# Kernel tuning notes

Hardware: AMD Instinct MI355X
Metric: run time of the kernel (lower is better)

Reference implementation:

```python
import jax, jax.numpy as jnp
import numpy as np

B, I, O, DEG = 16384, 1024, 1024, 8

def setup_inputs() -> dict:
    key = jax.random.key(0)
    kx, kc = jax.random.split(key)
    x = jax.random.normal(kx, (B, I), dtype=jnp.float32)
    std = 1.0 / (I * (DEG + 1))
    cheby_coeffs = jax.random.normal(kc, (I, O, DEG + 1), dtype=jnp.float32) * std
    return {"x": x, "cheby_coeffs": cheby_coeffs}


def reference(x, cheby_coeffs):
    # Chebyshev basis: T_d(tanh(x)) = cos(d * acos(tanh(x)))
    deg = cheby_coeffs.shape[-1]
    arange = jnp.arange(deg, dtype=x.dtype)  # (D+1,)
    theta = jnp.arccos(jnp.tanh(x))          # (B, I)
    basis = jnp.cos(theta[:, :, None] * arange)  # (B, I, D+1)
    y = jnp.einsum('bid,iod->bo', basis, cheby_coeffs)
    return y
```

## Files before the change

### kernel.cpp

```cpp
#include <hip/hip_runtime.h>
#include <hip/hip_bf16.h>


#define WSCALE 4096.0f
#define INV_WSCALE (1.0f/4096.0f)

typedef _Float16 f16;
typedef __fp16   hf2  __attribute__((ext_vector_type(2)));
typedef _Float16 f16x2v __attribute__((ext_vector_type(2)));
typedef _Float16 f16x8 __attribute__((ext_vector_type(8)));
typedef float    f32x4 __attribute__((ext_vector_type(4)));
typedef float    f32x4u __attribute__((ext_vector_type(4), aligned(4)));
typedef float    f32x2u __attribute__((ext_vector_type(2), aligned(4)));
typedef float    f32x16 __attribute__((ext_vector_type(16)));

union F16x8u { hf2 h2[4]; f16x8 v8; };

__global__ __launch_bounds__(256) void prep_kernel(const float* __restrict__ x,
                                                   const float* __restrict__ cc,
                                                   f16* __restrict__ t2,
                                                   f16* __restrict__ wt,
                                                   float* __restrict__ bias) {
  __shared__ char smem[18432];
  const int bid = blockIdx.x;
  const int t   = threadIdx.x;

  if (bid < 1024) {
    f16* s16 = (f16*)smem;
    const int u    = bid & 3;
    const int ncol = (bid >> 2) & 7;
    const int ic   = bid >> 5;
    const int i2   = t >> 4;
    const int o2   = t & 15;
    const int i0   = i2 * 2, o0 = o2 * 2;
    const int h    = i0 >> 4;
    const int kl   = (i0 >> 3) & 1;
    const int e    = i0 & 7;

    float va[2][18];
#pragma unroll
    for (int ii = 0; ii < 2; ++ii) {
      const float* g = cc + ((size_t)(ic * 32 + i0 + ii) * 1024
                             + (ncol * 128 + u * 32 + o0)) * 9;
      f32x4u a = *(const f32x4u*)(g);
      f32x4u b = *(const f32x4u*)(g + 4);
      f32x4u c4 = *(const f32x4u*)(g + 8);
      f32x4u d4 = *(const f32x4u*)(g + 12);
      f32x2u e2 = *(const f32x2u*)(g + 16);
#pragma unroll
      for (int j = 0; j < 4; ++j) { va[ii][j] = a[j]; va[ii][4 + j] = b[j];
                                    va[ii][8 + j] = c4[j]; va[ii][12 + j] = d4[j]; }
      va[ii][16] = e2[0]; va[ii][17] = e2[1];
    }

#pragma unroll
    for (int oo = 0; oo < 2; ++oo) {
      const int ol = o0 + oo;
      const int r  = ol & 15, q = ol >> 4;
      const int rk = (r >> 1) & 3;
      const int vsl = (kl * 2 + q) ^ rk;
      const int jj = h * 16 + r;
#pragma unroll
      for (int d = 0; d < 9; ++d) {
        f16x2v pv = { (f16)(va[0][oo * 9 + d] * WSCALE),
                      (f16)(va[1][oo * 9 + d] * WSCALE) };
        *(f16x2v*)(&s16[(d * 128 + jj * 4 + vsl) * 8 + e]) = pv;
      }
    }
    __syncthreads();

#pragma unroll
    for (int w = 0; w < 5; ++w) {
      int cidx = t + 256 * w;
      if (cidx < 1152) {
        f16x8 val = *(const f16x8*)(&s16[cidx * 8]);
        int d = cidx >> 7, rem = cidx & 127;
        *(f16x8*)(wt + (size_t)((d * 32 + ic) * 8 + ncol) * 4096 + u * 1024 + rem * 8) = val;
      }
    }
  } else if (bid < 1088) {
    float* red = (float*)smem;
    const int ol = t >> 4;
    const int sl = t & 15;
    const int o  = (bid - 1024) * 16 + ol;
    float s = 0.f;
    const float* p = cc + (size_t)(sl * 64) * 9216 + (size_t)o * 9;
#pragma unroll 4
    for (int i = 0; i < 64; ++i) s += p[(size_t)i * 9216];
    red[t] = s;
    __syncthreads();
    if (sl < 8) red[t] += red[t + 8];
    __syncthreads();
    if (sl < 4) red[t] += red[t + 4];
    __syncthreads();
    if (sl < 2) red[t] += red[t + 2];
    __syncthreads();
    if (sl == 0) bias[o] = red[t] + red[t + 1];
  } else {
    size_t gid = (size_t)(bid - 1088) * 256 + t;
    const float* p = x + gid * 8;
    f32x4 a = *(const f32x4*)p;
    f32x4 b = *(const f32x4*)(p + 4);
    float tf[8];
#pragma unroll
    for (int e = 0; e < 8; ++e) {
      float xx = (e < 4) ? a[e] : b[e - 4];
      tf[e] = 1.f - 2.f * __builtin_amdgcn_rcpf(__expf(2.f * xx) + 1.f);
    }
    F16x8u u;
#pragma unroll
    for (int q = 0; q < 4; ++q)
      u.h2[q] = __builtin_amdgcn_cvt_pkrtz(tf[2 * q], tf[2 * q + 1]);
    f16x8 v = u.v8 + u.v8;
    *(f16x8*)(t2 + gid * 8) = v;
  }
}

__global__ __launch_bounds__(256, 3) void cheby_gemm(const f16* __restrict__ t2g,
                                                     const f16* __restrict__ wt,
                                                     const float* __restrict__ bias,
                                                     float* __restrict__ out) {
  __shared__ f16 bbuf[5][4096];

  const int tid  = threadIdx.x;
  const int wid  = tid >> 6;
  const int lane = tid & 63;
  const int lr   = lane & 31;
  const int lh   = lane >> 5;
  const int wm   = wid >> 1;
  const int wn   = wid & 1;
  const int mrow = blockIdx.x >> 3;
  const int ncol = blockIdx.x & 7;
  const int m0   = mrow * 128 + wm * 64;
  const int n0   = ncol * 128 + wn * 64;
  const int rbase = wn * 2048 + ((lane & 15) * 4 + ((lane >> 4) ^ ((lane >> 1) & 3))) * 8;

  auto stage = [&](int cn, int dn, int slot) {
    const f16* src = wt + (size_t)(dn * 32 + cn) * 32768 + (size_t)ncol * 4096;
    __builtin_amdgcn_global_load_lds(
        (const __attribute__((address_space(1))) unsigned*)(src + tid * 8),
        (__attribute__((address_space(3))) unsigned*)(&bbuf[slot][wid * 512]),
        16, 0, 0);
    __builtin_amdgcn_global_load_lds(
        (const __attribute__((address_space(1))) unsigned*)(src + 2048 + tid * 8),
        (__attribute__((address_space(3))) unsigned*)(&bbuf[slot][wid * 512 + 2048]),
        16, 0, 0);
  };

  f32x16 acc[2][2];
#pragma unroll
  for (int a = 0; a < 2; ++a)
#pragma unroll
    for (int b = 0; b < 2; ++b)
#pragma unroll
      for (int j = 0; j < 16; ++j) acc[a][b][j] = 0.f;

  const f16x8 ones  = {(f16)1,(f16)1,(f16)1,(f16)1,(f16)1,(f16)1,(f16)1,(f16)1};
  const f16x8 half8 = {(f16)0.5f,(f16)0.5f,(f16)0.5f,(f16)0.5f,
                       (f16)0.5f,(f16)0.5f,(f16)0.5f,(f16)0.5f};
  f16x8 t2v[2][2], t2n[2][2];

  auto loadx = [&](int cn) {
#pragma unroll
    for (int mb = 0; mb < 2; ++mb)
#pragma unroll
      for (int h = 0; h < 2; ++h)
        t2n[mb][h] = *(const f16x8*)(t2g + (size_t)(m0 + mb * 32 + lr) * 1024
                                         + cn * 32 + h * 16 + lh * 8);
  };

#define REC(NEW, S1, S2)                                                       \
  _Pragma("unroll") for (int mb = 0; mb < 2; ++mb)                             \
    _Pragma("unroll") for (int h = 0; h < 2; ++h)                              \
      NEW[mb][h] = __builtin_elementwise_fma(t2v[mb][h], S1[mb][h], -S2[mb][h]);

#define LB(BD, SLOT)                                                           \
  {                                                                            \
    const f16* bb = &bbuf[0][0] + (SLOT) * 4096 + rbase;                       \
    BD[0][0] = *(const f16x8*)&bb[0];    BD[0][1] = *(const f16x8*)&bb[512];   \
    BD[1][0] = *(const f16x8*)&bb[1024]; BD[1][1] = *(const f16x8*)&bb[1536];  \
  }

#define M8(AF, BD)                                                             \
  {                                                                            \
    _Pragma("unroll") for (int nb = 0; nb < 2; ++nb)                           \
      _Pragma("unroll") for (int mb = 0; mb < 2; ++mb) {                       \
        acc[mb][nb] = __builtin_amdgcn_mfma_f32_32x32x16_f16(AF[mb][0], BD[nb][0], \
                                                             acc[mb][nb], 0, 0, 0); \
        acc[mb][nb] = __builtin_amdgcn_mfma_f32_32x32x16_f16(AF[mb][1], BD[nb][1], \
                                                             acc[mb][nb], 0, 0, 0); \
      }                                                                        \
  }

#define ADOPT                                                                  \
  _Pragma("unroll") for (int mb = 0; mb < 2; ++mb)                             \
    _Pragma("unroll") for (int h = 0; h < 2; ++h) {                            \
      t2v[mb][h] = t2n[mb][h];                                                 \
      A1[mb][h]  = t2v[mb][h] * half8;                                         \
    }

#define VMB(N)                                                                 \
  asm volatile("s_waitcnt vmcnt(" #N ")" ::: "memory");                        \
  __builtin_amdgcn_s_barrier();

  f16x8 onesA[2][2];
#pragma unroll
  for (int mb = 0; mb < 2; ++mb)
#pragma unroll
    for (int h = 0; h < 2; ++h) onesA[mb][h] = ones;

  f16x8 bfA[2][2], bfB[2][2];
  f16x8 A1[2][2], A2[2][2], A3[2][2], A4[2][2], A5[2][2], A6[2][2], A7[2][2], A8[2][2];
  int s1 = 0, s2 = 1, s3 = 2, s4 = 3, s5 = 4;

  loadx(0);
  stage(0, 1, s1); stage(0, 2, s2); stage(0, 3, s3); stage(0, 4, s4);

  for (int c = 0; c < 31; ++c) {
    VMB(4)
    LB(bfA, s1)
    ADOPT
    stage(c, 5, s5);
    loadx(c + 1);
    LB(bfB, s2)
    M8(A1, bfA)

    VMB(8) stage(c, 6, s1); LB(bfA, s3) REC(A2, A1, onesA) M8(A2, bfB)
    VMB(8) stage(c, 7, s2); LB(bfB, s4) REC(A3, A2, A1)    M8(A3, bfA)
    VMB(8) stage(c, 8, s3); LB(bfA, s5) REC(A4, A3, A2)    M8(A4, bfB)
    VMB(4) stage(c + 1, 1, s4); LB(bfB, s1) REC(A5, A4, A3) M8(A5, bfA)
    VMB(4) stage(c + 1, 2, s5); LB(bfA, s2) REC(A6, A5, A4) M8(A6, bfB)
    VMB(4) stage(c + 1, 3, s1); LB(bfB, s3) REC(A7, A6, A5) M8(A7, bfA)
    stage(c + 1, 4, s2);
    REC(A8, A7, A6) M8(A8, bfB)

    { int n1 = s4, n2 = s5, n3 = s1, n4 = s2, n5 = s3;
      s1 = n1; s2 = n2; s3 = n3; s4 = n4; s5 = n5; }
  }

  {
    VMB(4)
    LB(bfA, s1)
    ADOPT
    stage(31, 5, s5);
    LB(bfB, s2)
    M8(A1, bfA)

    VMB(4) stage(31, 6, s1); LB(bfA, s3) REC(A2, A1, onesA) M8(A2, bfB)
    VMB(4) stage(31, 7, s2); LB(bfB, s4) REC(A3, A2, A1)    M8(A3, bfA)
    VMB(4) stage(31, 8, s3); LB(bfA, s5) REC(A4, A3, A2)    M8(A4, bfB)
    VMB(4) LB(bfB, s1) REC(A5, A4, A3) M8(A5, bfA)
    VMB(2) LB(bfA, s2) REC(A6, A5, A4) M8(A6, bfB)
    VMB(0) LB(bfB, s3) REC(A7, A6, A5) M8(A7, bfA)
    REC(A8, A7, A6) M8(A8, bfB)
  }
#undef REC
#undef LB
#undef M8
#undef ADOPT
#undef VMB

  float bno[2];
  bno[0] = bias[n0 + lr];
  bno[1] = bias[n0 + 32 + lr];
#pragma unroll
  for (int mb = 0; mb < 2; ++mb)
#pragma unroll
    for (int nb = 0; nb < 2; ++nb)
#pragma unroll
      for (int j = 0; j < 16; ++j) {
        int row = m0 + mb * 32 + 4 * lh + (j & 3) + 8 * (j >> 2);
        int col = n0 + nb * 32 + lr;
        out[(size_t)row * 1024 + col] = acc[mb][nb][j] * INV_WSCALE + bno[nb];
      }
}

__global__ __launch_bounds__(512, 2) void cheby_gemm_fb(const float* __restrict__ x,
                                                        const f16* __restrict__ wt,
                                                        float* __restrict__ out) {
  __shared__ f16 bbuf[18][4096];
  const int tid  = threadIdx.x;
  const int wid  = tid >> 6;
  const int lane = tid & 63;
  const int lr   = lane & 31;
  const int lh   = lane >> 5;
  const int wm   = wid >> 1;
  const int wn   = wid & 1;
  const int mrow = blockIdx.x >> 3;
  const int ncol = blockIdx.x & 7;
  const int m0   = mrow * 256 + wm * 64;
  const int n0   = ncol * 128 + wn * 64;
  const int rbase = wn * 2048 + ((lane & 15) * 4 + ((lane >> 4) ^ ((lane >> 1) & 3))) * 8;

  auto stage = [&](int cn, int dn, int buf) {
    const f16* src = wt + (size_t)(dn * 32 + cn) * 32768 + (size_t)ncol * 4096;
    __builtin_amdgcn_global_load_lds(
        (const __attribute__((address_space(1))) unsigned*)(src + tid * 8),
        (__attribute__((address_space(3))) unsigned*)(&bbuf[buf][wid * 512]),
        16, 0, 0);
  };
  auto stage9 = [&](int cn, int b0) {
#pragma unroll
    for (int d = 0; d < 9; ++d) stage(cn, d, b0 + d);
  };

  f32x16 acc[2][2];
#pragma unroll
  for (int a = 0; a < 2; ++a)
#pragma unroll
    for (int b = 0; b < 2; ++b)
#pragma unroll
      for (int j = 0; j < 16; ++j) acc[a][b][j] = 0.f;

  const f16x8 ones  = {(f16)1,(f16)1,(f16)1,(f16)1,(f16)1,(f16)1,(f16)1,(f16)1};
  const f16x8 half8 = {(f16)0.5f,(f16)0.5f,(f16)0.5f,(f16)0.5f,
                       (f16)0.5f,(f16)0.5f,(f16)0.5f,(f16)0.5f};
  f16x8 t2v[2][2], t2n[2][2];
  f32x4 xf[2][2][2];

  auto loadx = [&](int cn) {
#pragma unroll
    for (int mb = 0; mb < 2; ++mb)
#pragma unroll
      for (int h = 0; h < 2; ++h) {
        const float* p = x + (size_t)(m0 + mb * 32 + lr) * 1024 + cn * 32 + h * 16 + lh * 8;
        xf[mb][h][0] = *(const f32x4*)p;
        xf[mb][h][1] = *(const f32x4*)(p + 4);
      }
  };
  auto dotanh = [&]() {
#pragma unroll
    for (int mb = 0; mb < 2; ++mb)
#pragma unroll
      for (int h = 0; h < 2; ++h) {
        float tf[8];
#pragma unroll
        for (int e = 0; e < 8; ++e) {
          float xx = (e < 4) ? xf[mb][h][0][e] : xf[mb][h][1][e - 4];
          tf[e] = 1.f - 2.f * __builtin_amdgcn_rcpf(__expf(2.f * xx) + 1.f);
        }
        F16x8u u;
#pragma unroll
        for (int q = 0; q < 4; ++q)
          u.h2[q] = __builtin_amdgcn_cvt_pkrtz(tf[2 * q], tf[2 * q + 1]);
        t2n[mb][h] = u.v8 + u.v8;
      }
  };

#define REC(NEW, S1, S2)                                                       \
  _Pragma("unroll") for (int mb = 0; mb < 2; ++mb)                             \
    _Pragma("unroll") for (int h = 0; h < 2; ++h)                              \
      NEW[mb][h] = __builtin_elementwise_fma(t2v[mb][h], S1[mb][h], -S2[mb][h]);
#define CLUSTER(AF, DIDX)                                                      \
  {                                                                            \
    const f16* bb = &bbuf[0][0] + sbase + (DIDX) * 4096 + rbase;               \
    f16x8 bf[2][2];                                                            \
    _Pragma("unroll") for (int nb = 0; nb < 2; ++nb)                           \
      _Pragma("unroll") for (int h = 0; h < 2; ++h)                            \
        bf[nb][h] = *(const f16x8*)&bb[nb * 1024 + h * 512];                   \
    _Pragma("unroll") for (int nb = 0; nb < 2; ++nb)                           \
      _Pragma("unroll") for (int mb = 0; mb < 2; ++mb) {                       \
        acc[mb][nb] = __builtin_amdgcn_mfma_f32_32x32x16_f16(AF[mb][0], bf[nb][0], \
                                                             acc[mb][nb], 0, 0, 0); \
        acc[mb][nb] = __builtin_amdgcn_mfma_f32_32x32x16_f16(AF[mb][1], bf[nb][1], \
                                                             acc[mb][nb], 0, 0, 0); \
      }                                                                        \
  }

  stage9(0, 0);
  loadx(0);
  dotanh();

  f16x8 onesA[2][2];
#pragma unroll
  for (int mb = 0; mb < 2; ++mb)
#pragma unroll
    for (int h = 0; h < 2; ++h) onesA[mb][h] = ones;

  for (int c = 0; c < 32; ++c) {
    const bool lastc = (c == 31);
    const int  sbase = (c & 1) * 36864;
    const int  nbase = (1 - (c & 1)) * 9;

    asm volatile("s_waitcnt vmcnt(8)" ::: "memory");
    __builtin_amdgcn_s_barrier();

    f16x8 A1[2][2], A2[2][2], A3[2][2], A4[2][2], A5[2][2], A6[2][2], A7[2][2], A8[2][2];
#pragma unroll
    for (int mb = 0; mb < 2; ++mb)
#pragma unroll
      for (int h = 0; h < 2; ++h) {
        t2v[mb][h] = t2n[mb][h];
        A1[mb][h]  = t2v[mb][h] * half8;
      }
    if (!lastc) { stage9(c + 1, nbase); loadx(c + 1); }

    CLUSTER(onesA, 0)
    CLUSTER(A1, 1)
    REC(A2, A1, onesA)  CLUSTER(A2, 2)
    REC(A3, A2, A1)     CLUSTER(A3, 3)
    REC(A4, A3, A2)     CLUSTER(A4, 4)
    REC(A5, A4, A3)     CLUSTER(A5, 5)
    REC(A6, A5, A4)     CLUSTER(A6, 6)
    REC(A7, A6, A5)     CLUSTER(A7, 7)
    REC(A8, A7, A6)     CLUSTER(A8, 8)
    if (!lastc) dotanh();
  }
#undef REC
#undef CLUSTER

#pragma unroll
  for (int mb = 0; mb < 2; ++mb)
#pragma unroll
    for (int nb = 0; nb < 2; ++nb)
#pragma unroll
      for (int j = 0; j < 16; ++j) {
        int row = m0 + mb * 32 + 4 * lh + (j & 3) + 8 * (j >> 2);
        int col = n0 + nb * 32 + lr;
        out[(size_t)row * 1024 + col] = acc[mb][nb][j] * INV_WSCALE;
      }
}

extern "C" void kernel_launch(void* const* d_in, const int* in_sizes, int n_in,
                              void* d_out, int out_size, void* d_ws, size_t ws_size,
                              hipStream_t stream) {
  const float* x  = (const float*)d_in[0];
  const float* cc = (const float*)d_in[1];
  f16*   wt   = (f16*)d_ws;
  f16*   t2   = (f16*)((char*)d_ws + 18874368);
  float* bias = (float*)((char*)d_ws + 52428800);
  float* out  = (float*)d_out;

  if (ws_size >= 52432896) {
    hipLaunchKernelGGL(prep_kernel, dim3(9280), dim3(256), 0, stream, x, cc, t2, wt, bias);
    hipLaunchKernelGGL(cheby_gemm, dim3(1024), dim3(256), 0, stream, t2, wt, bias, out);
  } else {
    hipLaunchKernelGGL(prep_kernel, dim3(1024), dim3(256), 0, stream, x, cc, t2, wt, bias);
    hipLaunchKernelGGL(cheby_gemm_fb, dim3(512), dim3(512), 0, stream, x, wt, out);
  }
}
```

Measured before the change: 284.6 us.

## Load B fragments directly from global memory, dropping LDS staging and barriers

Removes the 5-slot LDS ring buffer filled by global_load_lds and the per-step vmcnt waits and barriers. Each wave now reads its pre-swizzled weight fragments straight from global memory into registers, and the x loads are issued late in the loop. This cuts LDS traffic and synchronization, but each pair of waves that share a column now loads the same weights redundantly through L2/L1. Global-load latency is now hidden only by the register double buffer instead of a multi-stage prefetch.

Result: slower. 330.6 us (+16.1%).

```diff
diff --git a/kernel.cpp b/kernel.cpp
--- a/kernel.cpp
+++ b/kernel.cpp
@@ -120,8 +120,6 @@
                                                      const f16* __restrict__ wt,
                                                      const float* __restrict__ bias,
                                                      float* __restrict__ out) {
-  __shared__ f16 bbuf[5][4096];
-
   const int tid  = threadIdx.x;
   const int wid  = tid >> 6;
   const int lane = tid & 63;
@@ -133,19 +131,8 @@
   const int ncol = blockIdx.x & 7;
   const int m0   = mrow * 128 + wm * 64;
   const int n0   = ncol * 128 + wn * 64;
-  const int rbase = wn * 2048 + ((lane & 15) * 4 + ((lane >> 4) ^ ((lane >> 1) & 3))) * 8;
-
-  auto stage = [&](int cn, int dn, int slot) {
-    const f16* src = wt + (size_t)(dn * 32 + cn) * 32768 + (size_t)ncol * 4096;
-    __builtin_amdgcn_global_load_lds(
-        (const __attribute__((address_space(1))) unsigned*)(src + tid * 8),
-        (__attribute__((address_space(3))) unsigned*)(&bbuf[slot][wid * 512]),
-        16, 0, 0);
-    __builtin_amdgcn_global_load_lds(
-        (const __attribute__((address_space(1))) unsigned*)(src + 2048 + tid * 8),
-        (__attribute__((address_space(3))) unsigned*)(&bbuf[slot][wid * 512 + 2048]),
-        16, 0, 0);
-  };
+  const f16* bsrc = wt + (size_t)ncol * 4096 + wn * 2048
+                    + ((lane & 15) * 4 + ((lane >> 4) ^ ((lane >> 1) & 3))) * 8;
 
   f32x16 acc[2][2];
 #pragma unroll
@@ -158,28 +145,28 @@
   const f16x8 ones  = {(f16)1,(f16)1,(f16)1,(f16)1,(f16)1,(f16)1,(f16)1,(f16)1};
   const f16x8 half8 = {(f16)0.5f,(f16)0.5f,(f16)0.5f,(f16)0.5f,
                        (f16)0.5f,(f16)0.5f,(f16)0.5f,(f16)0.5f};
-  f16x8 t2v[2][2], t2n[2][2];
+  f16x8 t2v[2][2];
 
   auto loadx = [&](int cn) {
 #pragma unroll
     for (int mb = 0; mb < 2; ++mb)
 #pragma unroll
       for (int h = 0; h < 2; ++h)
-        t2n[mb][h] = *(const f16x8*)(t2g + (size_t)(m0 + mb * 32 + lr) * 1024
+        t2v[mb][h] = *(const f16x8*)(t2g + (size_t)(m0 + mb * 32 + lr) * 1024
                                          + cn * 32 + h * 16 + lh * 8);
   };
+
+#define LBG(BD, D, C)                                                          \
+  {                                                                            \
+    const f16* p = bsrc + (size_t)((D) * 32 + (C)) * 32768;                    \
+    BD[0][0] = *(const f16x8*)(p);        BD[0][1] = *(const f16x8*)(p + 512); \
+    BD[1][0] = *(const f16x8*)(p + 1024); BD[1][1] = *(const f16x8*)(p + 1536);\
+  }
 
 #define REC(NEW, S1, S2)                                                       \
   _Pragma("unroll") for (int mb = 0; mb < 2; ++mb)                             \
     _Pragma("unroll") for (int h = 0; h < 2; ++h)                              \
       NEW[mb][h] = __builtin_elementwise_fma(t2v[mb][h], S1[mb][h], -S2[mb][h]);
-
-#define LB(BD, SLOT)                                                           \
-  {                                                                            \
-    const f16* bb = &bbuf[0][0] + (SLOT) * 4096 + rbase;                       \
-    BD[0][0] = *(const f16x8*)&bb[0];    BD[0][1] = *(const f16x8*)&bb[512];   \
-    BD[1][0] = *(const f16x8*)&bb[1024]; BD[1][1] = *(const f16x8*)&bb[1536];  \
-  }
 
 #define M8(AF, BD)                                                             \
   {                                                                            \
@@ -192,17 +179,6 @@
       }                                                                        \
   }
 
-#define ADOPT                                                                  \
-  _Pragma("unroll") for (int mb = 0; mb < 2; ++mb)                             \
-    _Pragma("unroll") for (int h = 0; h < 2; ++h) {                            \
-      t2v[mb][h] = t2n[mb][h];                                                 \
-      A1[mb][h]  = t2v[mb][h] * half8;                                         \
-    }
-
-#define VMB(N)                                                                 \
-  asm volatile("s_waitcnt vmcnt(" #N ")" ::: "memory");                        \
-  __builtin_amdgcn_s_barrier();
-
   f16x8 onesA[2][2];
 #pragma unroll
   for (int mb = 0; mb < 2; ++mb)
@@ -211,54 +187,32 @@
 
   f16x8 bfA[2][2], bfB[2][2];
   f16x8 A1[2][2], A2[2][2], A3[2][2], A4[2][2], A5[2][2], A6[2][2], A7[2][2], A8[2][2];
-  int s1 = 0, s2 = 1, s3 = 2, s4 = 3, s5 = 4;
-
+
+  LBG(bfA, 1, 0)
   loadx(0);
-  stage(0, 1, s1); stage(0, 2, s2); stage(0, 3, s3); stage(0, 4, s4);
-
-  for (int c = 0; c < 31; ++c) {
-    VMB(4)
-    LB(bfA, s1)
-    ADOPT
-    stage(c, 5, s5);
-    loadx(c + 1);
-    LB(bfB, s2)
-    M8(A1, bfA)
-
-    VMB(8) stage(c, 6, s1); LB(bfA, s3) REC(A2, A1, onesA) M8(A2, bfB)
-    VMB(8) stage(c, 7, s2); LB(bfB, s4) REC(A3, A2, A1)    M8(A3, bfA)
-    VMB(8) stage(c, 8, s3); LB(bfA, s5) REC(A4, A3, A2)    M8(A4, bfB)
-    VMB(4) stage(c + 1, 1, s4); LB(bfB, s1) REC(A5, A4, A3) M8(A5, bfA)
-    VMB(4) stage(c + 1, 2, s5); LB(bfA, s2) REC(A6, A5, A4) M8(A6, bfB)
-    VMB(4) stage(c + 1, 3, s1); LB(bfB, s3) REC(A7, A6, A5) M8(A7, bfA)
-    stage(c + 1, 4, s2);
-    REC(A8, A7, A6) M8(A8, bfB)
-
-    { int n1 = s4, n2 = s5, n3 = s1, n4 = s2, n5 = s3;
-      s1 = n1; s2 = n2; s3 = n3; s4 = n4; s5 = n5; }
-  }
-
-  {
-    VMB(4)
-    LB(bfA, s1)
-    ADOPT
-    stage(31, 5, s5);
-    LB(bfB, s2)
-    M8(A1, bfA)
-
-    VMB(4) stage(31, 6, s1); LB(bfA, s3) REC(A2, A1, onesA) M8(A2, bfB)
-    VMB(4) stage(31, 7, s2); LB(bfB, s4) REC(A3, A2, A1)    M8(A3, bfA)
-    VMB(4) stage(31, 8, s3); LB(bfA, s5) REC(A4, A3, A2)    M8(A4, bfB)
-    VMB(4) LB(bfB, s1) REC(A5, A4, A3) M8(A5, bfA)
-    VMB(2) LB(bfA, s2) REC(A6, A5, A4) M8(A6, bfB)
-    VMB(0) LB(bfB, s3) REC(A7, A6, A5) M8(A7, bfA)
-    REC(A8, A7, A6) M8(A8, bfB)
-  }
+
+  for (int c = 0; c < 32; ++c) {
+    const int cn = (c < 31) ? c + 1 : 31;
+
+#pragma unroll
+    for (int mb = 0; mb < 2; ++mb)
+#pragma unroll
+      for (int h = 0; h < 2; ++h) A1[mb][h] = t2v[mb][h] * half8;
+
+    LBG(bfB, 2, c)                          M8(A1, bfA)
+    LBG(bfA, 3, c)  REC(A2, A1, onesA)      M8(A2, bfB)
+    LBG(bfB, 4, c)  REC(A3, A2, A1)         M8(A3, bfA)
+    LBG(bfA, 5, c)  REC(A4, A3, A2)         M8(A4, bfB)
+    LBG(bfB, 6, c)  REC(A5, A4, A3)         M8(A5, bfA)
+    LBG(bfA, 7, c)  REC(A6, A5, A4)         M8(A6, bfB)
+    LBG(bfB, 8, c)  REC(A7, A6, A5)         M8(A7, bfA)
+    LBG(bfA, 1, cn) REC(A8, A7, A6)
+    if (c < 31) loadx(c + 1);
+    M8(A8, bfB)
+  }
+#undef LBG
 #undef REC
-#undef LB
 #undef M8
-#undef ADOPT
-#undef VMB
 
   float bno[2];
   bno[0] = bias[n0 + lr];
```
